# Kernel optimization log

Measured on AMD Instinct MI355X. Metric: run time of the kernel, lower is better.

Reference implementation:

```python
import jax, jax.numpy as jnp
import numpy as np
from jax import lax

B, N, C = 4, 16384, 128
HEADS = 2
SR = 4
EPS = 1e-6


def setup_inputs() -> dict:
    key = jax.random.key(0)
    ks = jax.random.split(key, 6)
    s = 0.02
    return {
        "x": jax.random.normal(ks[0], (B, N, C), jnp.float32),
        "Wq": jax.random.normal(ks[1], (C, C), jnp.float32) * s,
        "Wk": jax.random.normal(ks[2], (C, C), jnp.float32) * s,
        "Wv": jax.random.normal(ks[3], (C, C), jnp.float32) * s,
        "Wproj": jax.random.normal(ks[4], (C, C), jnp.float32) * s,
        "sr_kernel": jax.random.normal(ks[5], (SR, SR, C, C), jnp.float32) * s,
        "sr_bias": jnp.zeros((C,), jnp.float32),
        "gamma": jnp.ones((C,), jnp.float32),
        "beta": jnp.zeros((C,), jnp.float32),
    }


def reference(x, Wq, Wk, Wv, Wproj, sr_kernel, sr_bias, gamma, beta):
    b, n, c = x.shape
    h = w = int(np.sqrt(n))          # H = W = sqrt(N), static
    dh = c // HEADS                  # head dim
    scale = dh ** -0.5

    # Q projection -> (B, heads, N, dh)
    q = (x @ Wq).reshape(b, n, HEADS, dh).transpose(0, 2, 1, 3)

    # Spatial reduction of K/V: conv stride=SR, 'same' padding, then LayerNorm
    x_img = x.reshape(b, h, w, c)
    x_ = lax.conv_general_dilated(
        x_img, sr_kernel, window_strides=(SR, SR), padding="SAME",
        dimension_numbers=("NHWC", "HWIO", "NHWC"))
    x_ = x_ + sr_bias
    x_ = x_.reshape(b, -1, c)        # (B, N', C), N' = (H/SR)*(W/SR)
    mu = jnp.mean(x_, axis=-1, keepdims=True)
    var = jnp.mean(jnp.square(x_ - mu), axis=-1, keepdims=True)
    x_ = (x_ - mu) * lax.rsqrt(var + EPS) * gamma + beta

    k = (x_ @ Wk).reshape(b, -1, HEADS, dh).transpose(0, 2, 1, 3)  # (B,h,N',dh)
    v = (x_ @ Wv).reshape(b, -1, HEADS, dh).transpose(0, 2, 1, 3)

    attn = jnp.einsum("bhqd,bhkd->bhqk", q, k) * scale
    attn = jax.nn.softmax(attn, axis=-1)
    out = jnp.einsum("bhqk,bhkd->bhqd", attn, v)
    out = out.transpose(0, 2, 1, 3).reshape(b, n, c)
    return out @ Wproj
```

## Files before the change

### kernel.cpp

```cpp
#include <hip/hip_runtime.h>
#include <hip/hip_bf16.h>

typedef unsigned short u16;
typedef __attribute__((ext_vector_type(8))) short short8;
typedef __attribute__((ext_vector_type(4))) float f32x4;
typedef __attribute__((ext_vector_type(2))) float f32x2;

#define MFMA16(a, b, c) __builtin_amdgcn_mfma_f32_16x16x32_bf16((a), (b), (c), 0, 0, 0)

__device__ __forceinline__ u16 f2bf(float f) {
  __hip_bfloat16 h = __float2bfloat16(f);
  u16 r;
  __builtin_memcpy(&r, &h, 2);
  return r;
}
__device__ __forceinline__ float bf2f(u16 h) {
  unsigned u = ((unsigned)h) << 16;
  float f;
  __builtin_memcpy(&f, &u, 4);
  return f;
}
__device__ __forceinline__ unsigned pk2(float a, float b) {
  unsigned r;
  asm("v_cvt_pk_bf16_f32 %0, %1, %2" : "=v"(r) : "v"(a), "v"(b));
  return r;
}
__device__ __forceinline__ short8 ld8(const void* src, int idx, int isf32) {
  short8 v;
  if (isf32) {
    const float4* s = (const float4*)((const float*)src + idx);
    float4 p0 = s[0], p1 = s[1];
    unsigned d0 = pk2(p0.x, p0.y), d1 = pk2(p0.z, p0.w);
    unsigned d2 = pk2(p1.x, p1.y), d3 = pk2(p1.z, p1.w);
    uint4 dd = {d0, d1, d2, d3};
    __builtin_memcpy(&v, &dd, 16);
  } else {
    v = *(const short8*)((const u16*)src + idx);
  }
  return v;
}
__device__ __forceinline__ float ld1(const void* src, int idx, int isf32) {
  return isf32 ? ((const float*)src)[idx] : bf2f(((const u16*)src)[idx]);
}
__device__ __forceinline__ int detect_isf32(const u16* xw) {
  int lane = threadIdx.x & 63;
  int cnt = 0;
#pragma unroll
  for (int i = 0; i < 16; ++i) {
    u16 w = xw[lane * 16 + i];
    cnt += (((w >> 7) & 0xFF) >= 0xC0) ? 1 : 0;
  }
#pragma unroll
  for (int off = 1; off < 64; off <<= 1) cnt += __shfl_xor(cnt, off, 64);
  return cnt >= 32;
}

__global__ void prep_kernel(const void* __restrict__ srk, const void* __restrict__ Wq,
                            const void* __restrict__ Wk, const void* __restrict__ Wv,
                            const void* __restrict__ Wp, const void* __restrict__ x,
                            u16* __restrict__ WcT) {
  const int isf32 = detect_isf32((const u16*)x);
  int gid = blockIdx.x * 256 + threadIdx.x;
  if (gid >= 327680) return;
  int cout = (gid >> 7) & 127, cin = gid & 127;
  float v;
  if (gid < 262144) {
    int mat = gid >> 14;
    v = ld1(srk, mat * 16384 + cin * 128 + cout, isf32);
  } else {
    int mat = (gid - 262144) >> 14;
    const void* src = (mat == 0) ? Wq : (mat == 1) ? Wk : (mat == 2) ? Wv : Wp;
    v = ld1(src, cin * 128 + cout, isf32);
  }
  WcT[gid] = f2bf(v);
}

__launch_bounds__(1024, 4)
__global__ void conv_ln_kv_kernel(const void* __restrict__ x, const u16* __restrict__ wcT,
                                  const void* __restrict__ sr_bias,
                                  const void* __restrict__ gamma,
                                  const void* __restrict__ beta,
                                  const u16* __restrict__ WkT, const u16* __restrict__ WvT,
                                  u16* __restrict__ Kb, u16* __restrict__ Vt) {
  extern __shared__ char cws[];
  float* Racc = (float*)cws;
  u16* Xs = (u16*)(cws + 16 * 16 * 128 * 4);
  const int isf32 = detect_isf32((const u16*)x);
  const int tid = threadIdx.x;
  const int wave = tid >> 6, lane = tid & 63;
  const int quad = lane >> 4, l16 = lane & 15;
  const int g = blockIdx.x;

  const int row = g * 16 + l16;
  const int pb = row >> 10, rem = row & 1023, oh = rem >> 5, ow = rem & 31;
  const int xbase = ((pb * 128 + oh * 4) * 128 + ow * 4) * 128;

  f32x4 acc[8];
#pragma unroll
  for (int i = 0; i < 8; ++i) acc[i] = (f32x4){0.f, 0.f, 0.f, 0.f};

  {
    const int r = wave >> 2, sc = wave & 3;
    short8 a[4];
#pragma unroll
    for (int kc = 0; kc < 4; ++kc)
      a[kc] = ld8(x, xbase + r * 16384 + sc * 128 + kc * 32 + quad * 8, isf32);
#pragma unroll
    for (int nt = 0; nt < 8; ++nt)
#pragma unroll
      for (int kc = 0; kc < 4; ++kc) {
        short8 bw = *(const short8*)(wcT + wave * 16384 + (nt * 16 + l16) * 128 +
                                     kc * 32 + quad * 8);
        acc[nt] = MFMA16(a[kc], bw, acc[nt]);
      }
  }
#pragma unroll
  for (int nt = 0; nt < 8; ++nt)
#pragma unroll
    for (int rr = 0; rr < 4; ++rr)
      Racc[(wave * 16 + quad * 4 + rr) * 128 + nt * 16 + l16] = acc[nt][rr];
  __syncthreads();

  {
    const int lrow = wave, c0 = lane * 2;
    f32x2 rsum = (f32x2){0.f, 0.f};
#pragma unroll
    for (int w = 0; w < 16; ++w) {
      f32x2 t = *(const f32x2*)&Racc[(w * 16 + lrow) * 128 + c0];
      rsum[0] += t[0];
      rsum[1] += t[1];
    }
    float v0 = rsum[0] + ld1(sr_bias, c0, isf32);
    float v1 = rsum[1] + ld1(sr_bias, c0 + 1, isf32);
    float sum = v0 + v1, sum2 = v0 * v0 + v1 * v1;
#pragma unroll
    for (int off = 1; off < 64; off <<= 1) {
      sum += __shfl_xor(sum, off, 64);
      sum2 += __shfl_xor(sum2, off, 64);
    }
    const float mu = sum * (1.f / 128.f);
    const float var = sum2 * (1.f / 128.f) - mu * mu;
    const float rinv = rsqrtf(fmaxf(var, 0.f) + 1e-6f);
    float y0 = (v0 - mu) * rinv * ld1(gamma, c0, isf32) + ld1(beta, c0, isf32);
    float y1 = (v1 - mu) * rinv * ld1(gamma, c0 + 1, isf32) + ld1(beta, c0 + 1, isf32);
    *(unsigned*)&Xs[lrow * 136 + c0] = pk2(y0, y1);
  }
  __syncthreads();

  short8 a2[4];
#pragma unroll
  for (int kc = 0; kc < 4; ++kc)
    a2[kc] = *(const short8*)&Xs[l16 * 136 + kc * 32 + quad * 8];
  const u16* Wm = (wave & 1) ? WvT : WkT;
  const int nt = wave >> 1;
  f32x4 a3 = (f32x4){0.f, 0.f, 0.f, 0.f};
#pragma unroll
  for (int kc = 0; kc < 4; ++kc) {
    short8 bm = *(const short8*)(Wm + (nt * 16 + l16) * 128 + kc * 32 + quad * 8);
    a3 = MFMA16(a2[kc], bm, a3);
  }
#pragma unroll
  for (int rr = 0; rr < 4; ++rr) {
    const int rowg = g * 16 + quad * 4 + rr;
    const int b = rowg >> 10, key = rowg & 1023;
    const int c = nt * 16 + l16;
    if (wave & 1)
      Vt[(b * 128 + c) * 1024 + key] = f2bf(a3[rr]);
    else
      Kb[rowg * 128 + c] = f2bf(a3[rr]);
  }
}

__launch_bounds__(512, 4)
__global__ void attn_kernel(const void* __restrict__ x, const u16* __restrict__ WqT,
                            const u16* __restrict__ WpT, const u16* __restrict__ Kb,
                            const u16* __restrict__ Vt, float* __restrict__ out) {
  extern __shared__ u16 lds[];
  u16* Ks = lds;
  u16* Vs = Ks + 64 * 136;
  u16* Pa = Vs + 128 * 72;
  const int isf32 = detect_isf32((const u16*)x);
  const int tid = threadIdx.x;
  const int wave = tid >> 6, lane = tid & 63;
  const int quad = lane >> 4, l16 = lane & 15;
  const int swz = (blockIdx.x & 7) * 64 + (blockIdx.x >> 3);
  const int b = swz >> 7;
  const int row0 = (swz & 127) * 128;
  const int wrow = wave * 16;
  u16* Pw = Pa + wave * 2176;

  const float qscale = 0.125f * 1.4426950408889634f;

  short8 qf[2][2];
  {
    short8 xb[4];
#pragma unroll
    for (int kc = 0; kc < 4; ++kc)
      xb[kc] = ld8(x, (b * 16384 + row0 + wrow + l16) * 128 + kc * 32 + quad * 8, isf32);
#pragma unroll
    for (int nt = 0; nt < 8; ++nt) {
      f32x4 qa = (f32x4){0.f, 0.f, 0.f, 0.f};
#pragma unroll
      for (int kc = 0; kc < 4; ++kc) {
        short8 w = *(const short8*)(WqT + (nt * 16 + l16) * 128 + kc * 32 + quad * 8);
        qa = MFMA16(w, xb[kc], qa);
      }
      uint2 pk = {pk2(qa[0] * qscale, qa[1] * qscale), pk2(qa[2] * qscale, qa[3] * qscale)};
      *(uint2*)&Pw[l16 * 136 + nt * 16 + quad * 4] = pk;
    }
#pragma unroll
    for (int h = 0; h < 2; ++h)
#pragma unroll
      for (int k0 = 0; k0 < 2; ++k0)
        qf[h][k0] = *(const short8*)&Pw[l16 * 136 + h * 64 + k0 * 32 + quad * 8];
  }

  f32x4 o[2][4];
#pragma unroll
  for (int h = 0; h < 2; ++h)
#pragma unroll
    for (int nt = 0; nt < 4; ++nt) o[h][nt] = (f32x4){0.f, 0.f, 0.f, 0.f};
  float l[2] = {0.f, 0.f};

  const int kkey = tid >> 3, kseg = tid & 7;
  const int vc = tid >> 2, vseg = tid & 3;

  for (int ch = 0; ch < 16; ++ch) {
    __syncthreads();
    {
      const uint4* src = (const uint4*)(Kb + (b * 1024 + ch * 64 + kkey) * 128 + kseg * 16);
      uint4* dst = (uint4*)&Ks[kkey * 136 + kseg * 16];
      dst[0] = src[0];
      dst[1] = src[1];
    }
    {
      const uint4* src = (const uint4*)(Vt + (b * 128 + vc) * 1024 + ch * 64 + vseg * 16);
      uint4* dst = (uint4*)&Vs[vc * 72 + vseg * 16];
      dst[0] = src[0];
      dst[1] = src[1];
    }
    __syncthreads();
#pragma unroll
    for (int h = 0; h < 2; ++h) {
#pragma unroll
      for (int ct = 0; ct < 4; ++ct) {
        short8 kf0 = *(const short8*)&Ks[(ct * 16 + l16) * 136 + h * 64 + quad * 8];
        short8 kf1 = *(const short8*)&Ks[(ct * 16 + l16) * 136 + h * 64 + 32 + quad * 8];
        f32x4 s0 = (f32x4){0.f, 0.f, 0.f, 0.f};
        s0 = MFMA16(kf0, qf[h][0], s0);
        s0 = MFMA16(kf1, qf[h][1], s0);
        float p0 = exp2f(s0[0]), p1 = exp2f(s0[1]), p2 = exp2f(s0[2]), p3 = exp2f(s0[3]);
        l[h] += (p0 + p1) + (p2 + p3);
        uint2 pka = {pk2(p0, p1), pk2(p2, p3)};
        *(uint2*)&Pw[l16 * 72 + ct * 16 + quad * 4] = pka;
      }
      __builtin_amdgcn_s_setprio(1);
#pragma unroll
      for (int kc = 0; kc < 2; ++kc) {
        short8 pf0 = *(const short8*)&Pw[l16 * 72 + kc * 32 + quad * 8];
#pragma unroll
        for (int nt = 0; nt < 4; ++nt) {
          short8 vf = *(const short8*)&Vs[(h * 64 + nt * 16 + l16) * 72 + kc * 32 + quad * 8];
          o[h][nt] = MFMA16(vf, pf0, o[h][nt]);
        }
      }
      __builtin_amdgcn_s_setprio(0);
    }
  }

#pragma unroll
  for (int h = 0; h < 2; ++h) {
    float t = l[h];
    t += __shfl_xor(t, 16, 64);
    t += __shfl_xor(t, 32, 64);
    const float inv = 1.0f / t;
#pragma unroll
    for (int nt = 0; nt < 4; ++nt)
#pragma unroll
      for (int rr = 0; rr < 4; ++rr) o[h][nt][rr] *= inv;
  }

  {
#pragma unroll
    for (int h = 0; h < 2; ++h)
#pragma unroll
      for (int nt = 0; nt < 4; ++nt) {
        uint2 pk = {pk2(o[h][nt][0], o[h][nt][1]), pk2(o[h][nt][2], o[h][nt][3])};
        *(uint2*)&Pw[l16 * 136 + h * 64 + nt * 16 + quad * 4] = pk;
      }
    short8 of[4];
#pragma unroll
    for (int kc = 0; kc < 4; ++kc)
      of[kc] = *(const short8*)&Pw[l16 * 136 + kc * 32 + quad * 8];
#pragma unroll
    for (int nt = 0; nt < 8; ++nt) {
      f32x4 pa = (f32x4){0.f, 0.f, 0.f, 0.f};
#pragma unroll
      for (int kc = 0; kc < 4; ++kc) {
        short8 w = *(const short8*)(WpT + (nt * 16 + l16) * 128 + kc * 32 + quad * 8);
        pa = MFMA16(of[kc], w, pa);
      }
#pragma unroll
      for (int rr = 0; rr < 4; ++rr)
        out[(b * 16384 + row0 + wrow + quad * 4 + rr) * 128 + nt * 16 + l16] = pa[rr];
    }
  }
}

extern "C" void kernel_launch(void* const* d_in, const int* in_sizes, int n_in,
                              void* d_out, int out_size, void* d_ws, size_t ws_size,
                              hipStream_t stream) {
  (void)in_sizes; (void)n_in; (void)out_size; (void)ws_size;
  const void* x = d_in[0];
  const void* Wq = d_in[1];
  const void* Wk = d_in[2];
  const void* Wv = d_in[3];
  const void* Wp = d_in[4];
  const void* srk = d_in[5];
  const void* sbias = d_in[6];
  const void* gamma = d_in[7];
  const void* beta = d_in[8];
  float* out = (float*)d_out;
  u16* ws = (u16*)d_ws;

  u16* WcT = ws;
  u16* WqT = ws + 262144;
  u16* WkT = ws + 278528;
  u16* WvT = ws + 294912;
  u16* WpT = ws + 311296;
  u16* Kb = ws + 327680;
  u16* Vt = ws + 851968;

  prep_kernel<<<dim3(1280), dim3(256), 0, stream>>>(srk, Wq, Wk, Wv, Wp, x, WcT);
  conv_ln_kv_kernel<<<dim3(256), dim3(1024), 16 * 16 * 128 * 4 + 16 * 136 * 2, stream>>>(
      x, WcT, sbias, gamma, beta, WkT, WvT, Kb, Vt);
  attn_kernel<<<dim3(512), dim3(512), (64 * 136 + 128 * 72 + 8 * 2176) * 2, stream>>>(
      x, WqT, WpT, Kb, Vt, out);
}
```

Before: 209.2 us.

## Switch attention to 32x32 MFMA tiles with 4 waves of 32 rows each

```diff
diff --git a/kernel.cpp b/kernel.cpp
--- a/kernel.cpp
+++ b/kernel.cpp
@@ -5,8 +5,10 @@
 typedef __attribute__((ext_vector_type(8))) short short8;
 typedef __attribute__((ext_vector_type(4))) float f32x4;
 typedef __attribute__((ext_vector_type(2))) float f32x2;
+typedef __attribute__((ext_vector_type(16))) float f32x16;
 
 #define MFMA16(a, b, c) __builtin_amdgcn_mfma_f32_16x16x32_bf16((a), (b), (c), 0, 0, 0)
+#define MFMA32(a, b, c) __builtin_amdgcn_mfma_f32_32x32x16_bf16((a), (b), (c), 0, 0, 0)
 
 __device__ __forceinline__ u16 f2bf(float f) {
   __hip_bfloat16 h = __float2bfloat16(f);
@@ -171,32 +173,35 @@
   }
 }
 
-__launch_bounds__(512, 4)
+__launch_bounds__(256, 4)
 __global__ void attn_kernel(const void* __restrict__ x, const u16* __restrict__ WqT,
                             const u16* __restrict__ WpT, const u16* __restrict__ Kb,
                             const u16* __restrict__ Vt, float* __restrict__ out) {
   extern __shared__ u16 lds[];
   u16* Ks = lds;
   u16* Vs = Ks + 64 * 136;
-  u16* Pa = Vs + 128 * 72;
+  u16* Pp = Vs + 128 * 72;
   const int isf32 = detect_isf32((const u16*)x);
   const int tid = threadIdx.x;
   const int wave = tid >> 6, lane = tid & 63;
   const int quad = lane >> 4, l16 = lane & 15;
+  const int q32 = lane & 31, hi = lane >> 5;
   const int swz = (blockIdx.x & 7) * 64 + (blockIdx.x >> 3);
   const int b = swz >> 7;
   const int row0 = (swz & 127) * 128;
-  const int wrow = wave * 16;
-  u16* Pw = Pa + wave * 2176;
+  const int wrow = wave * 32;
+  u16* Pw = Pp + wave * 2304;
+  u16* Fw = lds + wave * 4352;
 
   const float qscale = 0.125f * 1.4426950408889634f;
 
-  short8 qf[2][2];
-  {
+#pragma unroll
+  for (int mt = 0; mt < 2; ++mt) {
     short8 xb[4];
 #pragma unroll
     for (int kc = 0; kc < 4; ++kc)
-      xb[kc] = ld8(x, (b * 16384 + row0 + wrow + l16) * 128 + kc * 32 + quad * 8, isf32);
+      xb[kc] = ld8(x, (b * 16384 + row0 + wrow + mt * 16 + l16) * 128 + kc * 32 + quad * 8,
+                   isf32);
 #pragma unroll
     for (int nt = 0; nt < 8; ++nt) {
       f32x4 qa = (f32x4){0.f, 0.f, 0.f, 0.f};
@@ -206,64 +211,81 @@
         qa = MFMA16(w, xb[kc], qa);
       }
       uint2 pk = {pk2(qa[0] * qscale, qa[1] * qscale), pk2(qa[2] * qscale, qa[3] * qscale)};
-      *(uint2*)&Pw[l16 * 136 + nt * 16 + quad * 4] = pk;
-    }
-#pragma unroll
-    for (int h = 0; h < 2; ++h)
-#pragma unroll
-      for (int k0 = 0; k0 < 2; ++k0)
-        qf[h][k0] = *(const short8*)&Pw[l16 * 136 + h * 64 + k0 * 32 + quad * 8];
-  }
-
-  f32x4 o[2][4];
+      *(uint2*)&Fw[(mt * 16 + l16) * 136 + nt * 16 + quad * 4] = pk;
+    }
+  }
+  short8 qf[2][4];
 #pragma unroll
   for (int h = 0; h < 2; ++h)
 #pragma unroll
-    for (int nt = 0; nt < 4; ++nt) o[h][nt] = (f32x4){0.f, 0.f, 0.f, 0.f};
+    for (int s = 0; s < 4; ++s)
+      qf[h][s] = *(const short8*)&Fw[q32 * 136 + h * 64 + s * 16 + hi * 8];
+
+  f32x16 o[2][2];
+#pragma unroll
+  for (int h = 0; h < 2; ++h)
+#pragma unroll
+    for (int dt = 0; dt < 2; ++dt)
+#pragma unroll
+      for (int r = 0; r < 16; ++r) o[h][dt][r] = 0.f;
   float l[2] = {0.f, 0.f};
 
-  const int kkey = tid >> 3, kseg = tid & 7;
-  const int vc = tid >> 2, vseg = tid & 3;
+  const int kkey = tid >> 2, kseg = tid & 3;
+  const int vc = tid >> 1, vseg = tid & 1;
 
   for (int ch = 0; ch < 16; ++ch) {
     __syncthreads();
     {
-      const uint4* src = (const uint4*)(Kb + (b * 1024 + ch * 64 + kkey) * 128 + kseg * 16);
-      uint4* dst = (uint4*)&Ks[kkey * 136 + kseg * 16];
+      const uint4* src = (const uint4*)(Kb + (b * 1024 + ch * 64 + kkey) * 128 + kseg * 32);
+      uint4* dst = (uint4*)&Ks[kkey * 136 + kseg * 32];
       dst[0] = src[0];
       dst[1] = src[1];
+      dst[2] = src[2];
+      dst[3] = src[3];
     }
     {
-      const uint4* src = (const uint4*)(Vt + (b * 128 + vc) * 1024 + ch * 64 + vseg * 16);
-      uint4* dst = (uint4*)&Vs[vc * 72 + vseg * 16];
+      const uint4* src = (const uint4*)(Vt + (b * 128 + vc) * 1024 + ch * 64 + vseg * 32);
+      uint4* dst = (uint4*)&Vs[vc * 72 + vseg * 32];
       dst[0] = src[0];
       dst[1] = src[1];
+      dst[2] = src[2];
+      dst[3] = src[3];
     }
     __syncthreads();
 #pragma unroll
     for (int h = 0; h < 2; ++h) {
 #pragma unroll
-      for (int ct = 0; ct < 4; ++ct) {
-        short8 kf0 = *(const short8*)&Ks[(ct * 16 + l16) * 136 + h * 64 + quad * 8];
-        short8 kf1 = *(const short8*)&Ks[(ct * 16 + l16) * 136 + h * 64 + 32 + quad * 8];
-        f32x4 s0 = (f32x4){0.f, 0.f, 0.f, 0.f};
-        s0 = MFMA16(kf0, qf[h][0], s0);
-        s0 = MFMA16(kf1, qf[h][1], s0);
-        float p0 = exp2f(s0[0]), p1 = exp2f(s0[1]), p2 = exp2f(s0[2]), p3 = exp2f(s0[3]);
-        l[h] += (p0 + p1) + (p2 + p3);
-        uint2 pka = {pk2(p0, p1), pk2(p2, p3)};
-        *(uint2*)&Pw[l16 * 72 + ct * 16 + quad * 4] = pka;
-      }
+      for (int kt = 0; kt < 2; ++kt) {
+        f32x16 S;
+#pragma unroll
+        for (int r = 0; r < 16; ++r) S[r] = 0.f;
+#pragma unroll
+        for (int s = 0; s < 4; ++s) {
+          short8 kf = *(const short8*)&Ks[(kt * 32 + q32) * 136 + h * 64 + s * 16 + hi * 8];
+          S = MFMA32(kf, qf[h][s], S);
+        }
+        float lh = 0.f;
+#pragma unroll
+        for (int rp = 0; rp < 8; ++rp) {
+          float p0 = exp2f(S[2 * rp]), p1 = exp2f(S[2 * rp + 1]);
+          lh += p0 + p1;
+          *(unsigned*)&Pw[q32 * 72 + kt * 32 + (rp >> 1) * 8 + hi * 4 + (rp & 1) * 2] =
+              pk2(p0, p1);
+        }
+        l[h] += lh;
+      }
+      short8 pf[4];
+#pragma unroll
+      for (int s = 0; s < 4; ++s)
+        pf[s] = *(const short8*)&Pw[q32 * 72 + s * 16 + hi * 8];
       __builtin_amdgcn_s_setprio(1);
 #pragma unroll
-      for (int kc = 0; kc < 2; ++kc) {
-        short8 pf0 = *(const short8*)&Pw[l16 * 72 + kc * 32 + quad * 8];
-#pragma unroll
-        for (int nt = 0; nt < 4; ++nt) {
-          short8 vf = *(const short8*)&Vs[(h * 64 + nt * 16 + l16) * 72 + kc * 32 + quad * 8];
-          o[h][nt] = MFMA16(vf, pf0, o[h][nt]);
+      for (int dt = 0; dt < 2; ++dt)
+#pragma unroll
+        for (int s = 0; s < 4; ++s) {
+          short8 vf = *(const short8*)&Vs[(h * 64 + dt * 32 + q32) * 72 + s * 16 + hi * 8];
+          o[h][dt] = MFMA32(vf, pf[s], o[h][dt]);
         }
-      }
       __builtin_amdgcn_s_setprio(0);
     }
   }
@@ -271,27 +293,31 @@
 #pragma unroll
   for (int h = 0; h < 2; ++h) {
     float t = l[h];
-    t += __shfl_xor(t, 16, 64);
     t += __shfl_xor(t, 32, 64);
     const float inv = 1.0f / t;
 #pragma unroll
-    for (int nt = 0; nt < 4; ++nt)
-#pragma unroll
-      for (int rr = 0; rr < 4; ++rr) o[h][nt][rr] *= inv;
-  }
-
-  {
-#pragma unroll
-    for (int h = 0; h < 2; ++h)
-#pragma unroll
-      for (int nt = 0; nt < 4; ++nt) {
-        uint2 pk = {pk2(o[h][nt][0], o[h][nt][1]), pk2(o[h][nt][2], o[h][nt][3])};
-        *(uint2*)&Pw[l16 * 136 + h * 64 + nt * 16 + quad * 4] = pk;
-      }
+    for (int dt = 0; dt < 2; ++dt)
+#pragma unroll
+      for (int r = 0; r < 16; ++r) o[h][dt][r] *= inv;
+  }
+
+  __syncthreads();
+
+#pragma unroll
+  for (int h = 0; h < 2; ++h)
+#pragma unroll
+    for (int dt = 0; dt < 2; ++dt)
+#pragma unroll
+      for (int rp = 0; rp < 8; ++rp) {
+        *(unsigned*)&Fw[q32 * 136 + h * 64 + dt * 32 + (rp >> 1) * 8 + hi * 4 +
+                        (rp & 1) * 2] = pk2(o[h][dt][2 * rp], o[h][dt][2 * rp + 1]);
+      }
+#pragma unroll
+  for (int mt = 0; mt < 2; ++mt) {
     short8 of[4];
 #pragma unroll
     for (int kc = 0; kc < 4; ++kc)
-      of[kc] = *(const short8*)&Pw[l16 * 136 + kc * 32 + quad * 8];
+      of[kc] = *(const short8*)&Fw[(mt * 16 + l16) * 136 + kc * 32 + quad * 8];
 #pragma unroll
     for (int nt = 0; nt < 8; ++nt) {
       f32x4 pa = (f32x4){0.f, 0.f, 0.f, 0.f};
@@ -302,7 +328,8 @@
       }
 #pragma unroll
       for (int rr = 0; rr < 4; ++rr)
-        out[(b * 16384 + row0 + wrow + quad * 4 + rr) * 128 + nt * 16 + l16] = pa[rr];
+        out[(b * 16384 + row0 + wrow + mt * 16 + quad * 4 + rr) * 128 + nt * 16 + l16] =
+            pa[rr];
     }
   }
 }
@@ -334,6 +361,6 @@
   prep_kernel<<<dim3(1280), dim3(256), 0, stream>>>(srk, Wq, Wk, Wv, Wp, x, WcT);
   conv_ln_kv_kernel<<<dim3(256), dim3(1024), 16 * 16 * 128 * 4 + 16 * 136 * 2, stream>>>(
       x, WcT, sbias, gamma, beta, WkT, WvT, Kb, Vt);
-  attn_kernel<<<dim3(512), dim3(512), (64 * 136 + 128 * 72 + 8 * 2176) * 2, stream>>>(
+  attn_kernel<<<dim3(512), dim3(256), (64 * 136 + 128 * 72 + 4 * 2304) * 2, stream>>>(
       x, WqT, WpT, Kb, Vt, out);
 }
```

After: 407.1 us. 94.6% more time.
